# Kernel tuning notes

Hardware: AMD Instinct MI355X
Metric: run time of the kernel (lower is better)

The kernel has to match this reference:

```python
import jax, jax.numpy as jnp
import numpy as np
import math

EMBED_DIM = 128
NUM_HEADS = 16
HEAD_DIM = EMBED_DIM // NUM_HEADS  # = 8 = n_wires of the quantum circuit


def setup_inputs() -> dict:
    key = jax.random.key(0)
    k1, k2, k3 = jax.random.split(key, 3)
    B, S = 4, 2048
    x = jax.random.normal(k1, (B, S, EMBED_DIM), dtype=jnp.float32)
    # shared trainable RX angles of the single q_layer (applied to every head)
    theta = jax.random.normal(k2, (HEAD_DIM,), dtype=jnp.float32)
    w_out = jax.random.normal(k3, (EMBED_DIM, EMBED_DIM), dtype=jnp.float32) / math.sqrt(EMBED_DIM)
    mask = jnp.ones((B, S), dtype=jnp.int32)
    return {"x": x, "theta": theta, "w_out": w_out, "mask": mask}


def quantum_linear(x_head, theta):
    # Circuit: RX(x_i) encode + RX(theta_i) on wire i, CNOT chain (i, i+1),
    # then <Z_j>. For product state |psi_i> = RX(phi_i)|0>, <Z_i> = cos(phi_i),
    # and the CNOT chain gives final <Z_j> = prod_{i<=j} cos(phi_i).
    phi = x_head + theta  # [..., D] broadcast over leading dims
    return jnp.cumprod(jnp.cos(phi), axis=-1)


def reference(x, theta, w_out, mask):
    B, S, E = x.shape
    H, D = NUM_HEADS, HEAD_DIM
    xs = x.reshape(B, S, H, D)
    q = quantum_linear(xs, theta).transpose(0, 2, 1, 3)  # [B, H, S, D]; k = v = q
    scores = jnp.einsum("bhsd,bhtd->bhst", q, q) / math.sqrt(D)
    scores = jnp.where(mask[:, None, None, :] == 0, -1e9, scores)
    probs = jax.nn.softmax(scores, axis=-1)  # dropout is identity in eval
    attn = jnp.einsum("bhst,bhtd->bhsd", probs, q)
    attn = attn.transpose(0, 2, 1, 3).reshape(B, S, E)
    return attn @ w_out.T
```

## Files before the change

kernel.cpp:

```cpp
#include <hip/hip_runtime.h>
#include <hip/hip_bf16.h>
#include <hip/hip_fp16.h>

#define NB 4
#define NS 2048
#define NE 128
#define NH 16
#define ND 8

typedef __attribute__((ext_vector_type(8))) _Float16 half8;
typedef __attribute__((ext_vector_type(4))) float f32x4;

#define VSTRIDE 2056
#define PSTRIDE 18

__device__ __forceinline__ unsigned int pkrtz(float a, float b) {
    typedef __fp16 fp16v2 __attribute__((ext_vector_type(2)));
    union { fp16v2 h; unsigned int u; } v;
    v.h = __builtin_amdgcn_cvt_pkrtz(a, b);
    return v.u;
}
__device__ __forceinline__ unsigned short f2h(float a) {
    return __half_as_ushort(__float2half(a));
}
__device__ __forceinline__ half8 ld_p(const unsigned int* p) {
    union { half8 s; unsigned int u[4]; } v;
    v.u[0] = p[0]; v.u[1] = p[1]; v.u[2] = p[2]; v.u[3] = p[3];
    return v.s;
}

__global__ __launch_bounds__(1024) void attn_kernel(
        const float* __restrict__ x,
        const float* __restrict__ theta,
        const int* __restrict__ mask,
        unsigned short* __restrict__ mid) {
    __shared__ unsigned short qhl[NS * ND];
    __shared__ unsigned short vT[9 * VSTRIDE];
    __shared__ unsigned int   Pu[16 * 2 * 16 * PSTRIDE];

    const int bid = blockIdx.x;
    const int bh = bid >> 2;
    const int b = bh >> 4, h = bh & (NH - 1);
    const int mquart = bid & 3;
    const int tid = threadIdx.x;

    const float SC = 0.71421629f;

    float th[ND];
#pragma unroll
    for (int d = 0; d < ND; d++) th[d] = theta[d];

    {
        int ch = tid >> 4, i = tid & 15;
        int t0 = ch * 32 + i, t1 = t0 + 16;
        float p0[ND], p1[ND];
        {
            const float* xp = x + ((size_t)(b * NS + t0) * NE + h * ND);
            float4 a = *(const float4*)xp, c = *(const float4*)(xp + 4);
            float p = 1.f;
            p *= cosf(a.x + th[0]); p0[0] = p; p *= cosf(a.y + th[1]); p0[1] = p;
            p *= cosf(a.z + th[2]); p0[2] = p; p *= cosf(a.w + th[3]); p0[3] = p;
            p *= cosf(c.x + th[4]); p0[4] = p; p *= cosf(c.y + th[5]); p0[5] = p;
            p *= cosf(c.z + th[6]); p0[6] = p; p *= cosf(c.w + th[7]); p0[7] = p;
        }
        {
            const float* xp = x + ((size_t)(b * NS + t1) * NE + h * ND);
            float4 a = *(const float4*)xp, c = *(const float4*)(xp + 4);
            float p = 1.f;
            p *= cosf(a.x + th[0]); p1[0] = p; p *= cosf(a.y + th[1]); p1[1] = p;
            p *= cosf(a.z + th[2]); p1[2] = p; p *= cosf(a.w + th[3]); p1[3] = p;
            p *= cosf(c.x + th[4]); p1[4] = p; p *= cosf(c.y + th[5]); p1[5] = p;
            p *= cosf(c.z + th[6]); p1[6] = p; p *= cosf(c.w + th[7]); p1[7] = p;
        }
        uint4 qa, qb;
        qa.x = pkrtz(p0[0] * SC, p0[1] * SC);
        qa.y = pkrtz(p0[2] * SC, p0[3] * SC);
        qa.z = pkrtz(p0[4] * SC, p0[5] * SC);
        qa.w = pkrtz(p0[6] * SC, p0[7] * SC);
        qb.x = pkrtz(p1[0] * SC, p1[1] * SC);
        qb.y = pkrtz(p1[2] * SC, p1[3] * SC);
        qb.z = pkrtz(p1[4] * SC, p1[5] * SC);
        qb.w = pkrtz(p1[6] * SC, p1[7] * SC);
        *(uint4*)&qhl[t0 * ND] = qa;
        *(uint4*)&qhl[t1 * ND] = qb;
#pragma unroll
        for (int d = 0; d < ND; d++)
            *(unsigned int*)&vT[d * VSTRIDE + ch * 32 + 2 * i] = pkrtz(p0[d], p1[d]);
        *(unsigned int*)&vT[8 * VSTRIDE + ch * 32 + 2 * i] = 0x3C003C00u;
    }
    __syncthreads();

    const int wave = tid >> 6, lane = tid & 63;
    const int quad = lane >> 4, l15 = lane & 15;
    const int mbase = mquart * 512 + wave * 32;

    half8 hz = {0, 0, 0, 0, 0, 0, 0, 0};
    half8 afrag[2];
#pragma unroll
    for (int mt = 0; mt < 2; mt++) {
        half8 a = *(const half8*)&qhl[(mbase + mt * 16 + l15) * ND];
        afrag[mt] = quad ? hz : a;
    }
    const int vrow = (l15 == 8) ? 8 : (l15 & 7);
    const unsigned short* vbase = &vT[vrow * VSTRIDE];
    const int* mrow = mask + b * NS;
    unsigned int* Pw0 = Pu + wave * (2 * 16 * PSTRIDE);
    unsigned int* Pw1 = Pw0 + 16 * PSTRIDE;

    f32x4 O0 = {0.f, 0.f, 0.f, 0.f}, O1 = {0.f, 0.f, 0.f, 0.f};
    for (int ch = 0; ch < 64; ch++) {
        int tb = ch * 32;
        half8 bf0 = *(const half8*)&qhl[(tb + l15) * ND];
        half8 bf1 = *(const half8*)&qhl[(tb + 16 + l15) * ND];
        half8 vf = *(const half8*)&vbase[tb + quad * 8];
        float bias0 = mrow[tb + l15] ? 0.f : -30000.f;
        float bias1 = mrow[tb + 16 + l15] ? 0.f : -30000.f;
        f32x4 B0 = {bias0, bias0, bias0, bias0};
        f32x4 B1 = {bias1, bias1, bias1, bias1};

        f32x4 c0 = __builtin_amdgcn_mfma_f32_16x16x32_f16(afrag[0], bf0, B0, 0, 0, 0);
        f32x4 c1 = __builtin_amdgcn_mfma_f32_16x16x32_f16(afrag[0], bf1, B1, 0, 0, 0);
        f32x4 d0 = __builtin_amdgcn_mfma_f32_16x16x32_f16(afrag[1], bf0, B0, 0, 0, 0);
        f32x4 d1 = __builtin_amdgcn_mfma_f32_16x16x32_f16(afrag[1], bf1, B1, 0, 0, 0);
#pragma unroll
        for (int r = 0; r < 4; r++) {
            float e0 = __builtin_amdgcn_exp2f(c0[r]);
            float e1 = __builtin_amdgcn_exp2f(c1[r]);
            Pw0[(quad * 4 + r) * PSTRIDE + l15] = pkrtz(e0, e1);
            float f0 = __builtin_amdgcn_exp2f(d0[r]);
            float f1 = __builtin_amdgcn_exp2f(d1[r]);
            Pw1[(quad * 4 + r) * PSTRIDE + l15] = pkrtz(f0, f1);
        }
        __asm__ volatile("" ::: "memory");
        half8 pf0 = ld_p(Pw0 + l15 * PSTRIDE + quad * 4);
        half8 pf1 = ld_p(Pw1 + l15 * PSTRIDE + quad * 4);
        O0 = __builtin_amdgcn_mfma_f32_16x16x32_f16(pf0, vf, O0, 0, 0, 0);
        O1 = __builtin_amdgcn_mfma_f32_16x16x32_f16(pf1, vf, O1, 0, 0, 0);
        __asm__ volatile("" ::: "memory");
    }

#pragma unroll
    for (int mt = 0; mt < 2; mt++) {
        f32x4 O = mt ? O1 : O0;
#pragma unroll
        for (int r = 0; r < 4; r++) {
            float lsum = __shfl(O[r], (lane & 48) | 8, 64);
            float v = O[r] / lsum;
            if (l15 < ND) {
                int m = mbase + mt * 16 + quad * 4 + r;
                mid[(size_t)(b * NS + m) * NE + h * ND + l15] = f2h(v);
            }
        }
    }
}

__global__ __launch_bounds__(256) void proj_kernel(
        const unsigned short* __restrict__ mid,
        const float* __restrict__ w,
        float* __restrict__ out) {
    __shared__ unsigned short wf[NE * 136];
    __shared__ unsigned short am[32 * 136];
    const int rb = blockIdx.x * 32;
    const int tid = threadIdx.x;

    for (int i = tid; i < 2048; i += 256) {
        const float* wp = w + i * 8;
        float4 a = *(const float4*)wp, c = *(const float4*)(wp + 4);
        uint4 pk;
        pk.x = pkrtz(a.x, a.y); pk.y = pkrtz(a.z, a.w);
        pk.z = pkrtz(c.x, c.y); pk.w = pkrtz(c.z, c.w);
        int n = i >> 4, k8 = (i & 15) * 8;
        *(uint4*)&wf[n * 136 + k8] = pk;
    }
    for (int i = tid; i < 512; i += 256) {
        int r = i >> 4, k8 = (i & 15) * 8;
        uint4 v = *(const uint4*)&mid[(size_t)(rb + r) * NE + k8];
        *(uint4*)&am[r * 136 + k8] = v;
    }
    __syncthreads();

    const int wave = tid >> 6, lane = tid & 63;
    const int quad = lane >> 4, l15 = lane & 15;
    const int mt = wave & 1, nh = wave >> 1;

    half8 af[4];
#pragma unroll
    for (int kt = 0; kt < 4; kt++)
        af[kt] = *(const half8*)&am[(mt * 16 + l15) * 136 + kt * 32 + quad * 8];

#pragma unroll
    for (int nt = 0; nt < 4; nt++) {
        int n0 = (nh * 4 + nt) * 16;
        f32x4 acc = {0.f, 0.f, 0.f, 0.f};
#pragma unroll
        for (int kt = 0; kt < 4; kt++) {
            half8 bf = *(const half8*)&wf[(n0 + l15) * 136 + kt * 32 + quad * 8];
            acc = __builtin_amdgcn_mfma_f32_16x16x32_f16(af[kt], bf, acc, 0, 0, 0);
        }
#pragma unroll
        for (int r = 0; r < 4; r++)
            out[(size_t)(rb + mt * 16 + quad * 4 + r) * NE + n0 + l15] = acc[r];
    }
}

extern "C" void kernel_launch(void* const* d_in, const int* in_sizes, int n_in,
                              void* d_out, int out_size, void* d_ws, size_t ws_size,
                              hipStream_t stream) {
    const float* x     = (const float*)d_in[0];
    const float* theta = (const float*)d_in[1];
    const float* w_out = (const float*)d_in[2];
    const int*   mask  = (const int*)d_in[3];
    float* out = (float*)d_out;

    unsigned short* mid16 = (unsigned short*)d_ws;

    attn_kernel<<<NB * NH * 4, 1024, 0, stream>>>(x, theta, mask, mid16);
    proj_kernel<<<NB * NS / 32, 256, 0, stream>>>(mid16, w_out, out);
}
```

Measured before the change: 112.8 us.

## Compute transposed scores so P feeds PV MFMA directly from registers

Computes the score tile as K·Q^T instead of Q·K^T, so each lane's accumulator rows line up with the A-operand layout of the following PV MFMA. The exponentiated probabilities are then packed into half8 fragments in registers, removing the per-iteration LDS round-trip through the P scratch buffer. Keys are permuted when written into shared memory so the packed key order matches the V layout, and the mask becomes a vectorized int4 load per row. The change depends on that permuted key layout and on padding qhl to guard the quad-offset reads, which adds some indexing complexity.

```diff
diff --git a/kernel.cpp b/kernel.cpp
--- a/kernel.cpp
+++ b/kernel.cpp
@@ -12,7 +12,6 @@
 typedef __attribute__((ext_vector_type(4))) float f32x4;
 
 #define VSTRIDE 2056
-#define PSTRIDE 18
 
 __device__ __forceinline__ unsigned int pkrtz(float a, float b) {
     typedef __fp16 fp16v2 __attribute__((ext_vector_type(2)));
@@ -23,10 +22,11 @@
 __device__ __forceinline__ unsigned short f2h(float a) {
     return __half_as_ushort(__float2half(a));
 }
-__device__ __forceinline__ half8 ld_p(const unsigned int* p) {
-    union { half8 s; unsigned int u[4]; } v;
-    v.u[0] = p[0]; v.u[1] = p[1]; v.u[2] = p[2]; v.u[3] = p[3];
-    return v.s;
+__device__ __forceinline__ half8 mk_half8(unsigned u0, unsigned u1,
+                                          unsigned u2, unsigned u3) {
+    union { half8 h; unsigned u[4]; } v;
+    v.u[0] = u0; v.u[1] = u1; v.u[2] = u2; v.u[3] = u3;
+    return v.h;
 }
 
 __global__ __launch_bounds__(1024) void attn_kernel(
@@ -34,9 +34,8 @@
         const float* __restrict__ theta,
         const int* __restrict__ mask,
         unsigned short* __restrict__ mid) {
-    __shared__ unsigned short qhl[NS * ND];
+    __shared__ unsigned short qhl[NS * ND + 24];
     __shared__ unsigned short vT[9 * VSTRIDE];
-    __shared__ unsigned int   Pu[16 * 2 * 16 * PSTRIDE];
 
     const int bid = blockIdx.x;
     const int bh = bid >> 2;
@@ -51,11 +50,12 @@
     for (int d = 0; d < ND; d++) th[d] = theta[d];
 
     {
-        int ch = tid >> 4, i = tid & 15;
-        int t0 = ch * 32 + i, t1 = t0 + 16;
+        int chs = tid >> 4, i = tid & 15;
+        int ta = 4 * (i >> 2) + 2 * (i & 1) + 16 * ((i >> 1) & 1);
+        int r0 = chs * 32 + ta, r1 = r0 + 1;
         float p0[ND], p1[ND];
         {
-            const float* xp = x + ((size_t)(b * NS + t0) * NE + h * ND);
+            const float* xp = x + ((size_t)(b * NS + r0) * NE + h * ND);
             float4 a = *(const float4*)xp, c = *(const float4*)(xp + 4);
             float p = 1.f;
             p *= cosf(a.x + th[0]); p0[0] = p; p *= cosf(a.y + th[1]); p0[1] = p;
@@ -64,7 +64,7 @@
             p *= cosf(c.z + th[6]); p0[6] = p; p *= cosf(c.w + th[7]); p0[7] = p;
         }
         {
-            const float* xp = x + ((size_t)(b * NS + t1) * NE + h * ND);
+            const float* xp = x + ((size_t)(b * NS + r1) * NE + h * ND);
             float4 a = *(const float4*)xp, c = *(const float4*)(xp + 4);
             float p = 1.f;
             p *= cosf(a.x + th[0]); p1[0] = p; p *= cosf(a.y + th[1]); p1[1] = p;
@@ -81,13 +81,14 @@
         qb.y = pkrtz(p1[2] * SC, p1[3] * SC);
         qb.z = pkrtz(p1[4] * SC, p1[5] * SC);
         qb.w = pkrtz(p1[6] * SC, p1[7] * SC);
-        *(uint4*)&qhl[t0 * ND] = qa;
-        *(uint4*)&qhl[t1 * ND] = qb;
+        *(uint4*)&qhl[r0 * ND] = qa;
+        *(uint4*)&qhl[r1 * ND] = qb;
 #pragma unroll
         for (int d = 0; d < ND; d++)
-            *(unsigned int*)&vT[d * VSTRIDE + ch * 32 + 2 * i] = pkrtz(p0[d], p1[d]);
-        *(unsigned int*)&vT[8 * VSTRIDE + ch * 32 + 2 * i] = 0x3C003C00u;
-    }
+            *(unsigned int*)&vT[d * VSTRIDE + chs * 32 + 2 * i] = pkrtz(p0[d], p1[d]);
+        *(unsigned int*)&vT[8 * VSTRIDE + chs * 32 + 2 * i] = 0x3C003C00u;
+    }
+    if (tid < 24) qhl[NS * ND + tid] = 0;
     __syncthreads();
 
     const int wave = tid >> 6, lane = tid & 63;
@@ -95,48 +96,44 @@
     const int mbase = mquart * 512 + wave * 32;
 
     half8 hz = {0, 0, 0, 0, 0, 0, 0, 0};
-    half8 afrag[2];
-#pragma unroll
-    for (int mt = 0; mt < 2; mt++) {
-        half8 a = *(const half8*)&qhl[(mbase + mt * 16 + l15) * ND];
-        afrag[mt] = quad ? hz : a;
-    }
-    const int vrow = (l15 == 8) ? 8 : (l15 & 7);
+    half8 bm0 = quad ? hz : *(const half8*)&qhl[(mbase + l15) * ND];
+    half8 bm1 = quad ? hz : *(const half8*)&qhl[(mbase + 16 + l15) * ND];
+
+    const int vrow = (l15 < 9) ? l15 : 8;
     const unsigned short* vbase = &vT[vrow * VSTRIDE];
     const int* mrow = mask + b * NS;
-    unsigned int* Pw0 = Pu + wave * (2 * 16 * PSTRIDE);
-    unsigned int* Pw1 = Pw0 + 16 * PSTRIDE;
 
     f32x4 O0 = {0.f, 0.f, 0.f, 0.f}, O1 = {0.f, 0.f, 0.f, 0.f};
     for (int ch = 0; ch < 64; ch++) {
         int tb = ch * 32;
-        half8 bf0 = *(const half8*)&qhl[(tb + l15) * ND];
-        half8 bf1 = *(const half8*)&qhl[(tb + 16 + l15) * ND];
-        half8 vf = *(const half8*)&vbase[tb + quad * 8];
-        float bias0 = mrow[tb + l15] ? 0.f : -30000.f;
-        float bias1 = mrow[tb + 16 + l15] ? 0.f : -30000.f;
-        f32x4 B0 = {bias0, bias0, bias0, bias0};
-        f32x4 B1 = {bias1, bias1, bias1, bias1};
-
-        f32x4 c0 = __builtin_amdgcn_mfma_f32_16x16x32_f16(afrag[0], bf0, B0, 0, 0, 0);
-        f32x4 c1 = __builtin_amdgcn_mfma_f32_16x16x32_f16(afrag[0], bf1, B1, 0, 0, 0);
-        f32x4 d0 = __builtin_amdgcn_mfma_f32_16x16x32_f16(afrag[1], bf0, B0, 0, 0, 0);
-        f32x4 d1 = __builtin_amdgcn_mfma_f32_16x16x32_f16(afrag[1], bf1, B1, 0, 0, 0);
-#pragma unroll
-        for (int r = 0; r < 4; r++) {
-            float e0 = __builtin_amdgcn_exp2f(c0[r]);
-            float e1 = __builtin_amdgcn_exp2f(c1[r]);
-            Pw0[(quad * 4 + r) * PSTRIDE + l15] = pkrtz(e0, e1);
-            float f0 = __builtin_amdgcn_exp2f(d0[r]);
-            float f1 = __builtin_amdgcn_exp2f(d1[r]);
-            Pw1[(quad * 4 + r) * PSTRIDE + l15] = pkrtz(f0, f1);
-        }
-        __asm__ volatile("" ::: "memory");
-        half8 pf0 = ld_p(Pw0 + l15 * PSTRIDE + quad * 4);
-        half8 pf1 = ld_p(Pw1 + l15 * PSTRIDE + quad * 4);
-        O0 = __builtin_amdgcn_mfma_f32_16x16x32_f16(pf0, vf, O0, 0, 0, 0);
-        O1 = __builtin_amdgcn_mfma_f32_16x16x32_f16(pf1, vf, O1, 0, 0, 0);
-        __asm__ volatile("" ::: "memory");
+        half8 at0 = *(const half8*)&qhl[(tb + l15) * ND + quad * 8];
+        half8 at1 = *(const half8*)&qhl[(tb + 16 + l15) * ND + quad * 8];
+        half8 vf  = *(const half8*)&vbase[tb + quad * 8];
+        int4 mk0 = *(const int4*)&mrow[tb + quad * 4];
+        int4 mk1 = *(const int4*)&mrow[tb + 16 + quad * 4];
+        f32x4 C0 = {mk0.x ? 0.f : -30000.f, mk0.y ? 0.f : -30000.f,
+                    mk0.z ? 0.f : -30000.f, mk0.w ? 0.f : -30000.f};
+        f32x4 C1 = {mk1.x ? 0.f : -30000.f, mk1.y ? 0.f : -30000.f,
+                    mk1.z ? 0.f : -30000.f, mk1.w ? 0.f : -30000.f};
+
+        f32x4 s00 = __builtin_amdgcn_mfma_f32_16x16x32_f16(at0, bm0, C0, 0, 0, 0);
+        f32x4 s01 = __builtin_amdgcn_mfma_f32_16x16x32_f16(at0, bm1, C0, 0, 0, 0);
+        f32x4 s10 = __builtin_amdgcn_mfma_f32_16x16x32_f16(at1, bm0, C1, 0, 0, 0);
+        f32x4 s11 = __builtin_amdgcn_mfma_f32_16x16x32_f16(at1, bm1, C1, 0, 0, 0);
+
+        half8 pA0 = mk_half8(
+            pkrtz(__builtin_amdgcn_exp2f(s00[0]), __builtin_amdgcn_exp2f(s00[1])),
+            pkrtz(__builtin_amdgcn_exp2f(s00[2]), __builtin_amdgcn_exp2f(s00[3])),
+            pkrtz(__builtin_amdgcn_exp2f(s10[0]), __builtin_amdgcn_exp2f(s10[1])),
+            pkrtz(__builtin_amdgcn_exp2f(s10[2]), __builtin_amdgcn_exp2f(s10[3])));
+        half8 pA1 = mk_half8(
+            pkrtz(__builtin_amdgcn_exp2f(s01[0]), __builtin_amdgcn_exp2f(s01[1])),
+            pkrtz(__builtin_amdgcn_exp2f(s01[2]), __builtin_amdgcn_exp2f(s01[3])),
+            pkrtz(__builtin_amdgcn_exp2f(s11[0]), __builtin_amdgcn_exp2f(s11[1])),
+            pkrtz(__builtin_amdgcn_exp2f(s11[2]), __builtin_amdgcn_exp2f(s11[3])));
+
+        O0 = __builtin_amdgcn_mfma_f32_16x16x32_f16(pA0, vf, O0, 0, 0, 0);
+        O1 = __builtin_amdgcn_mfma_f32_16x16x32_f16(pA1, vf, O1, 0, 0, 0);
     }
 
 #pragma unroll
```

After: 110.9 us. Within noise of the previous version (-1.7%).
